# Performance work log

Measured on AMD Instinct MI355X. Metric: run time of the kernel, lower is better.

Reference implementation:

```python
import jax, jax.numpy as jnp
import numpy as np

T = 200                      # TRAIN_ROIS_PER_IMAGE
RATIO = 0.33                 # ROI_POSITIVE_RATIO
P_MAX = int(T * RATIO)       # max positive ROIs (66)
MH, MW = 28, 28              # MASK_SHAPE
STD = jnp.array([0.1, 0.1, 0.2, 0.2], jnp.float32)  # BBOX_STD_DEV
EPS = 1e-6


def _iou(a, b):
    # a [N,4], b [G,4] -> [N,G] IoU (same math as overlaps_graph, without tiling)
    ay1, ax1, ay2, ax2 = a[:, 0:1], a[:, 1:2], a[:, 2:3], a[:, 3:4]
    by1, bx1, by2, bx2 = b[None, :, 0], b[None, :, 1], b[None, :, 2], b[None, :, 3]
    iy = jnp.maximum(jnp.minimum(ay2, by2) - jnp.maximum(ay1, by1), 0.0)
    ix = jnp.maximum(jnp.minimum(ax2, bx2) - jnp.maximum(ax1, bx1), 0.0)
    inter = iy * ix
    union = (ay2 - ay1) * (ax2 - ax1) + (by2 - by1) * (bx2 - bx1) - inter
    return inter / jnp.maximum(union, EPS)


def _box_refinement(box, gt):
    # standard Mask R-CNN box_refinement_graph
    h = jnp.maximum(box[:, 2] - box[:, 0], EPS)
    w = jnp.maximum(box[:, 3] - box[:, 1], EPS)
    cy = box[:, 0] + 0.5 * h
    cx = box[:, 1] + 0.5 * w
    gh = jnp.maximum(gt[:, 2] - gt[:, 0], EPS)
    gw = jnp.maximum(gt[:, 3] - gt[:, 1], EPS)
    gcy = gt[:, 0] + 0.5 * gh
    gcx = gt[:, 1] + 0.5 * gw
    return jnp.stack([(gcy - cy) / h, (gcx - cx) / w,
                      jnp.log(gh / h), jnp.log(gw / w)], axis=-1)


def _crop_and_resize(imgs, boxes):
    # imgs [T,H,W], boxes [T,4] normalized; TF crop_and_resize bilinear semantics,
    # extrapolation_value = 0 for samples outside [0, H-1] x [0, W-1].
    Tn, H, W = imgs.shape
    y1, x1, y2, x2 = boxes[:, 0], boxes[:, 1], boxes[:, 2], boxes[:, 3]
    iy = jnp.arange(MH, dtype=jnp.float32)
    ix = jnp.arange(MW, dtype=jnp.float32)
    ys = y1[:, None] * (H - 1) + iy[None, :] * ((y2 - y1) * (H - 1) / (MH - 1))[:, None]  # [T,MH]
    xs = x1[:, None] * (W - 1) + ix[None, :] * ((x2 - x1) * (W - 1) / (MW - 1))[:, None]  # [T,MW]
    y0 = jnp.floor(ys); x0 = jnp.floor(xs)
    wy = (ys - y0)[:, :, None]
    wx = (xs - x0)[:, None, :]
    y0i = jnp.clip(y0, 0, H - 1).astype(jnp.int32)
    y1i = jnp.clip(y0 + 1, 0, H - 1).astype(jnp.int32)
    x0i = jnp.clip(x0, 0, W - 1).astype(jnp.int32)
    x1i = jnp.clip(x0 + 1, 0, W - 1).astype(jnp.int32)
    t = jnp.arange(Tn)[:, None, None]
    v00 = imgs[t, y0i[:, :, None], x0i[:, None, :]]
    v01 = imgs[t, y0i[:, :, None], x1i[:, None, :]]
    v10 = imgs[t, y1i[:, :, None], x0i[:, None, :]]
    v11 = imgs[t, y1i[:, :, None], x1i[:, None, :]]
    val = (v00 * (1 - wx) + v01 * wx) * (1 - wy) + (v10 * (1 - wx) + v11 * wx) * wy
    ok = ((ys >= 0) & (ys <= H - 1))[:, :, None] & ((xs >= 0) & (xs <= W - 1))[:, None, :]
    return jnp.where(ok, val, 0.0)


def _targets_one(proposals, class_ids, boxes, masks):
    # proposals [N,4], class_ids [G] int, boxes [G,4], masks [H,W,G]
    N = proposals.shape[0]
    # zero-padding trim expressed as validity masks (jit-friendly fixed shapes)
    valid_prop = jnp.any(proposals != 0, axis=1)
    valid_gt = jnp.any(boxes != 0, axis=1)
    non_crowd = (class_ids > 0) & valid_gt
    crowd = (class_ids < 0) & valid_gt

    ov = _iou(proposals, boxes)                              # [N,G]
    ov_nc = jnp.where(non_crowd[None, :], ov, -1.0)          # mask crowd/padded gt
    roi_iou_max = ov_nc.max(axis=1)
    crowd_max = jnp.where(crowd[None, :], ov, 0.0).max(axis=1)

    pos_mask = valid_prop & (roi_iou_max >= 0.5)
    neg_mask = valid_prop & (roi_iou_max < 0.5) & (crowd_max < 0.001)

    # deterministic selection (original uses tf.random.shuffle): positives first-in-order
    pos_order = jnp.argsort(jnp.where(pos_mask, 0, 1))
    neg_order = jnp.argsort(jnp.where(neg_mask, 0, 1))
    pos_count = jnp.minimum(pos_mask.sum(), P_MAX)
    neg_needed = jnp.floor(pos_count.astype(jnp.float32) / RATIO).astype(jnp.int32) - pos_count
    neg_count = jnp.minimum(jnp.minimum(neg_needed, neg_mask.sum()), T - pos_count)

    slot = jnp.arange(T)
    is_pos = slot < pos_count
    is_neg = (slot >= pos_count) & (slot < pos_count + neg_count)
    src = jnp.where(is_pos,
                    pos_order[jnp.clip(slot, 0, N - 1)],
                    neg_order[jnp.clip(slot - pos_count, 0, N - 1)])
    rois = jnp.where((is_pos | is_neg)[:, None], proposals[src], 0.0)

    assign = jnp.argmax(ov_nc[src], axis=1)                  # gt assignment per slot
    gt_box = boxes[assign]
    gt_cls = jnp.where(is_pos, class_ids[assign], 0)

    deltas = _box_refinement(rois, gt_box) / STD
    deltas = jnp.where(is_pos[:, None], deltas, 0.0)

    # USE_MINI_MASK: roi box in gt-box-normalized coordinates
    gy1, gx1, gy2, gx2 = gt_box[:, 0], gt_box[:, 1], gt_box[:, 2], gt_box[:, 3]
    gh = jnp.maximum(gy2 - gy1, EPS)
    gw = jnp.maximum(gx2 - gx1, EPS)
    mm = jnp.stack([(rois[:, 0] - gy1) / gh, (rois[:, 1] - gx1) / gw,
                    (rois[:, 2] - gy1) / gh, (rois[:, 3] - gx1) / gw], axis=-1)

    roi_masks = jnp.moveaxis(jnp.take(masks, assign, axis=2), 2, 0)  # [T,H,W]
    m = jnp.round(_crop_and_resize(roi_masks, mm))
    m = jnp.where(is_pos[:, None, None], m, 0.0)
    return rois, gt_cls, deltas, m


def setup_inputs() -> dict:
    key = jax.random.key(0)
    ks = jax.random.split(key, 4)
    B, N, G, HM = 16, 2000, 200, 56

    def boxes_of(k, shape):
        k1, k2, k3, k4 = jax.random.split(k, 4)
        y1 = jax.random.uniform(k1, shape) * 0.5
        x1 = jax.random.uniform(k2, shape) * 0.5
        h = 0.1 + jax.random.uniform(k3, shape) * 0.4
        w = 0.1 + jax.random.uniform(k4, shape) * 0.4
        return jnp.stack([y1, x1, y1 + h, x1 + w], axis=-1)

    proposals = boxes_of(ks[0], (B, N))
    proposals = proposals * (jnp.arange(N) < N - 200)[None, :, None]  # zero-padded tail
    prior_class_ids = jax.random.randint(ks[1], (B, G), -1, 81).astype(jnp.int32)  # -1=crowd, 0=padding
    prior_boxes = boxes_of(ks[2], (B, G)) * (prior_class_ids != 0)[..., None]
    prior_masks = (jax.random.uniform(ks[3], (B, HM, HM, G)) > 0.5).astype(jnp.float32)
    return {"proposals": proposals, "prior_class_ids": prior_class_ids,
            "prior_boxes": prior_boxes, "prior_masks": prior_masks}


def reference(proposals, prior_class_ids, prior_boxes, prior_masks):
    rois, cls, deltas, masks = jax.vmap(_targets_one)(proposals, prior_class_ids,
                                                      prior_boxes, prior_masks)
    return rois, cls, deltas, masks
```

## Files before the change

kernel.cpp:

```cpp
#include <hip/hip_runtime.h>
#include <math.h>

#pragma clang fp contract(off)

#define BN     16
#define NP     2000
#define NG     200
#define NT     200
#define PMAX   66
#define EPSF   1e-6f
#define MH     28
#define MW     28
#define HM     56
#define NPIX   (HM*HM)
#define NPLANE 66

__global__ __launch_bounds__(256) void kA(
    const float* __restrict__ proposals, const int* __restrict__ cls_ids,
    const float* __restrict__ boxes,
    int* __restrict__ flag_ws, int* __restrict__ assign_ws)
{
#pragma clang fp contract(off)
  const int b = blockIdx.y;
  __shared__ float4 gbox[NG];
  __shared__ float  garea[NG];
  __shared__ int    gflag[NG];

  for (int j = threadIdx.x; j < NG; j += 256) {
    float4 g = reinterpret_cast<const float4*>(boxes + (size_t)b * NG * 4)[j];
    int c = cls_ids[b * NG + j];
    bool vg = (g.x != 0.f) || (g.y != 0.f) || (g.z != 0.f) || (g.w != 0.f);
    gbox[j]  = g;
    garea[j] = (g.z - g.x) * (g.w - g.y);
    gflag[j] = vg ? (c > 0 ? 1 : (c < 0 ? 2 : 0)) : 0;
  }
  __syncthreads();

  int i = blockIdx.x * 256 + threadIdx.x;
  if (i >= NP) return;

  float4 p = reinterpret_cast<const float4*>(proposals + (size_t)b * NP * 4)[i];
  bool vp = (p.x != 0.f) || (p.y != 0.f) || (p.z != 0.f) || (p.w != 0.f);
  float pa = (p.z - p.x) * (p.w - p.y);

  float best = -3.0e38f;
  int   bestj = 0;
  float cmax = 0.f;
  for (int j = 0; j < NG; ++j) {
    float4 g = gbox[j];
    float iy = fmaxf(fminf(p.z, g.z) - fmaxf(p.x, g.x), 0.f);
    float ix = fmaxf(fminf(p.w, g.w) - fmaxf(p.y, g.y), 0.f);
    float inter = iy * ix;
    float uni = (pa + garea[j]) - inter;
    float iou = inter / fmaxf(uni, EPSF);
    int fl = gflag[j];
    float v = (fl == 1) ? iou : -1.0f;
    if (v > best) { best = v; bestj = j; }
    if (fl == 2) cmax = fmaxf(cmax, iou);
  }
  bool pos = vp && (best >= 0.5f);
  bool neg = vp && (best < 0.5f) && (cmax < 0.001f);
  flag_ws[b * NP + i]   = pos ? 1 : (neg ? 2 : 0);
  assign_ws[b * NP + i] = bestj;
}

__global__ __launch_bounds__(256) void kB(
    const float* __restrict__ proposals, const int* __restrict__ cls_ids,
    const float* __restrict__ boxes, const int* __restrict__ flag_ws,
    const int* __restrict__ assign_ws, float* __restrict__ out,
    float* __restrict__ mm_ws, int* __restrict__ pa_ws,
    int* __restrict__ gmap_ws)
{
#pragma clang fp contract(off)
  const int b = blockIdx.x;
  const int tid = threadIdx.x;
  const int lane = tid & 63;
  const int wv = tid >> 6;

  __shared__ unsigned short pos_list[NP];
  __shared__ unsigned short neg_list[NP];
  __shared__ int wcp[4], wcn[4];
  __shared__ int s_pt, s_nt;
  __shared__ int used[NG];
  __shared__ int gplane[NG];
  __shared__ int wtot[4];
  if (tid == 0) { s_pt = 0; s_nt = 0; }
  __syncthreads();

  const int* fb = flag_ws + b * NP;
  for (int base = 0; base < NP; base += 256) {
    int i = base + tid;
    int f = (i < NP) ? fb[i] : 0;
    bool isp = (f == 1), isn = (f == 2);
    unsigned long long bp = __ballot(isp);
    unsigned long long bn = __ballot(isn);
    __syncthreads();
    if (lane == 0) { wcp[wv] = __popcll(bp); wcn[wv] = __popcll(bn); }
    __syncthreads();
    int prep = __popcll(bp & ((1ull << lane) - 1ull));
    int pren = __popcll(bn & ((1ull << lane) - 1ull));
    int bpp = 0, bnn = 0, tp = 0, tn = 0;
    for (int w = 0; w < 4; ++w) {
      if (w < wv) { bpp += wcp[w]; bnn += wcn[w]; }
      tp += wcp[w]; tn += wcn[w];
    }
    int pt = s_pt, nt = s_nt;
    if (isp) pos_list[pt + bpp + prep] = (unsigned short)i;
    if (isn) neg_list[nt + bnn + pren] = (unsigned short)i;
    __syncthreads();
    if (tid == 0) { s_pt = pt + tp; s_nt = nt + tn; }
  }
  __syncthreads();

  int pos_total = s_pt, neg_total = s_nt;
  int pos_count = min(pos_total, PMAX);
  int neg_needed = (int)floorf((float)pos_count / 0.33f) - pos_count;
  int neg_count = min(min(neg_needed, neg_total), NT - pos_count);

  for (int j = tid; j < NG; j += 256) used[j] = 0;
  __syncthreads();

  int ma = -1;
  if (tid < NT) {
    bool ispos = tid < pos_count;
    bool isneg = (!ispos) && (tid < pos_count + neg_count);
    float r0 = 0.f, r1 = 0.f, r2 = 0.f, r3 = 0.f;
    float d0 = 0.f, d1 = 0.f, d2 = 0.f, d3 = 0.f;
    float m0 = 0.f, m1 = 0.f, m2 = 0.f, m3 = 0.f;
    float clsf = 0.f;
    if (ispos || isneg) {
      int i = ispos ? (int)pos_list[tid] : (int)neg_list[tid - pos_count];
      float4 p = reinterpret_cast<const float4*>(proposals + (size_t)b * NP * 4)[i];
      r0 = p.x; r1 = p.y; r2 = p.z; r3 = p.w;
      if (ispos) {
        int a = assign_ws[b * NP + i];
        ma = a;
        used[a] = 1;
        float4 g = reinterpret_cast<const float4*>(boxes + (size_t)b * NG * 4)[a];
        float h  = fmaxf(r2 - r0, EPSF);
        float w  = fmaxf(r3 - r1, EPSF);
        float cy = r0 + 0.5f * h;
        float cx = r1 + 0.5f * w;
        float gh = fmaxf(g.z - g.x, EPSF);
        float gw = fmaxf(g.w - g.y, EPSF);
        float gcy = g.x + 0.5f * gh;
        float gcx = g.y + 0.5f * gw;
        d0 = ((gcy - cy) / h) / 0.1f;
        d1 = ((gcx - cx) / w) / 0.1f;
        d2 = logf(gh / h) / 0.2f;
        d3 = logf(gw / w) / 0.2f;
        m0 = (r0 - g.x) / gh;
        m1 = (r1 - g.y) / gw;
        m2 = (r2 - g.x) / gh;
        m3 = (r3 - g.y) / gw;
        clsf = (float)cls_ids[b * NG + a];
      }
    }
    int s = b * NT + tid;
    float* rois = out;
    float* cls  = out + BN * NT * 4;
    float* dlt  = out + BN * NT * 4 + BN * NT;
    rois[s * 4 + 0] = r0; rois[s * 4 + 1] = r1;
    rois[s * 4 + 2] = r2; rois[s * 4 + 3] = r3;
    cls[s] = clsf;
    dlt[s * 4 + 0] = d0; dlt[s * 4 + 1] = d1;
    dlt[s * 4 + 2] = d2; dlt[s * 4 + 3] = d3;
    mm_ws[s * 4 + 0] = m0; mm_ws[s * 4 + 1] = m1;
    mm_ws[s * 4 + 2] = m2; mm_ws[s * 4 + 3] = m3;
  }
  __syncthreads();

  {
    int j = tid;
    int u = (j < NG) ? used[j] : 0;
    unsigned long long m = __ballot(u != 0);
    int pre = __popcll(m & ((1ull << lane) - 1ull));
    if (lane == 0) wtot[wv] = __popcll(m);
    __syncthreads();
    int basep = 0;
    for (int w = 0; w < wv; ++w) basep += wtot[w];
    if (j < NG) {
      int pl = u ? (basep + pre) : -1;
      gplane[j] = pl;
      gmap_ws[b * NG + j] = pl;
    }
  }
  __syncthreads();

  if (tid < NT)
    pa_ws[b * NT + tid] = (ma >= 0) ? gplane[ma] : -1;
}

__global__ __launch_bounds__(256) void kG(
    const float* __restrict__ masks, const int* __restrict__ gmap_ws,
    float* __restrict__ staged)
{
  const int b  = blockIdx.y;
  const int p0 = blockIdx.x * 64;
  const int tid = threadIdx.x;
  __shared__ float tile[64][65];
  __shared__ int   splane[64];
  __shared__ int   s_any;

  const float* mbase = masks + (size_t)b * NPIX * NG;

  for (int gc = 0; gc < NG; gc += 64) {
    if (tid < 64)
      splane[tid] = (gc + tid < NG) ? gmap_ws[b * NG + gc + tid] : -1;
    if (tid == 0) s_any = 0;
    __syncthreads();
    if (tid < 64 && splane[tid] >= 0) s_any = 1;
    __syncthreads();
    if (s_any) {
      for (int e = 0; e < 16; ++e) {
        int idx = e * 256 + tid;
        int gl  = idx & 63;
        int pl  = idx >> 6;
        int g   = gc + gl;
        float v = 0.f;
        if (g < NG) v = mbase[(size_t)(p0 + pl) * NG + g];
        tile[gl][pl] = v;
      }
      __syncthreads();
      for (int e = 0; e < 16; ++e) {
        int idx = e * 256 + tid;
        int pl  = idx & 63;
        int gl  = idx >> 6;
        int plane = splane[gl];
        if (plane >= 0)
          staged[(size_t)(b * NPLANE + plane) * NPIX + (p0 + pl)] = tile[gl][pl];
      }
    }
    __syncthreads();
  }
}

__global__ __launch_bounds__(256) void kC(
    const float* __restrict__ staged, const float* __restrict__ mm_ws,
    const int* __restrict__ pa_ws, float* __restrict__ out)
{
#pragma clang fp contract(off)
  const int s = blockIdx.x;
  float4* om = reinterpret_cast<float4*>(
      out + (size_t)(BN * NT * 9) + (size_t)s * (MH * MW));
  const int q = threadIdx.x;
  if (q >= (MH * MW) / 4) return;
  int pa = pa_ws[s];
  if (pa < 0) { om[q] = make_float4(0.f, 0.f, 0.f, 0.f); return; }

  const int b = s / NT;
  float y1 = mm_ws[s * 4 + 0], x1 = mm_ws[s * 4 + 1];
  float y2 = mm_ws[s * 4 + 2], x2 = mm_ws[s * 4 + 3];
  float sy = (y2 - y1) * 55.0f / 27.0f;
  float sx = (x2 - x1) * 55.0f / 27.0f;
  const float* mp = staged + (size_t)(b * NPLANE + pa) * NPIX;

  int px0 = q * 4;
  int my  = px0 / MW;
  float ys = y1 * 55.0f + (float)my * sy;
  float y0f = floorf(ys);
  float wy  = ys - y0f;
  int y0i = (int)fminf(fmaxf(y0f, 0.f), 55.f);
  int y1i = (int)fminf(fmaxf(y0f + 1.0f, 0.f), 55.f);
  bool oky = (ys >= 0.f) && (ys <= 55.f);
  const float* r0 = mp + y0i * HM;
  const float* r1 = mp + y1i * HM;

  float res[4];
  for (int k = 0; k < 4; ++k) {
    int mx = (px0 + k) - my * MW;
    float xs = x1 * 55.0f + (float)mx * sx;
    float x0f = floorf(xs);
    float wx  = xs - x0f;
    int x0i = (int)fminf(fmaxf(x0f, 0.f), 55.f);
    int x1i = (int)fminf(fmaxf(x0f + 1.0f, 0.f), 55.f);
    float v00 = r0[x0i], v01 = r0[x1i];
    float v10 = r1[x0i], v11 = r1[x1i];
    float val = (v00 * (1.f - wx) + v01 * wx) * (1.f - wy)
              + (v10 * (1.f - wx) + v11 * wx) * wy;
    bool ok = oky && (xs >= 0.f) && (xs <= 55.f);
    res[k] = ok ? rintf(val) : 0.f;
  }
  om[q] = make_float4(res[0], res[1], res[2], res[3]);
}

extern "C" void kernel_launch(void* const* d_in, const int* in_sizes, int n_in,
                              void* d_out, int out_size, void* d_ws, size_t ws_size,
                              hipStream_t stream)
{
  const float* proposals = (const float*)d_in[0];
  const int*   cls_ids   = (const int*)d_in[1];
  const float* boxes     = (const float*)d_in[2];
  const float* masks     = (const float*)d_in[3];
  float* out = (float*)d_out;

  char* ws = (char*)d_ws;
  int*   flag_ws   = (int*)ws;    ws += (size_t)BN * NP * sizeof(int);
  int*   assign_ws = (int*)ws;    ws += (size_t)BN * NP * sizeof(int);
  float* mm_ws     = (float*)ws;  ws += (size_t)BN * NT * 4 * sizeof(float);
  int*   pa_ws     = (int*)ws;    ws += (size_t)BN * NT * sizeof(int);
  int*   gmap_ws   = (int*)ws;    ws += (size_t)BN * NG * sizeof(int);
  float* staged    = (float*)ws;

  dim3 gA((NP + 255) / 256, BN);
  kA<<<gA, 256, 0, stream>>>(proposals, cls_ids, boxes, flag_ws, assign_ws);
  kB<<<BN, 256, 0, stream>>>(proposals, cls_ids, boxes, flag_ws, assign_ws,
                             out, mm_ws, pa_ws, gmap_ws);
  dim3 gG(NPIX / 64, BN);
  kG<<<gG, 256, 0, stream>>>(masks, gmap_ws, staged);
  kC<<<BN * NT, 256, 0, stream>>>(staged, mm_ws, pa_ws, out);
}
```

Baseline: 140.1 us.

## Rewrite mask gather with float4 row loads and compact used-plane list

The mask staging kernel now loads each 64-pixel row block of all 200 ground-truth mask values with float4 loads into a single shared tile. It then writes out only the used planes, taken from a compact list built from the plane map and a per-image used count that the selection kernel now records. This replaces the earlier loop over 64-wide GT chunks with transposes and repeated syncs. A second change lets the IoU kernel return early for zero-padded proposals. The tile is large (about 52 KB of shared memory) and the whole row block is always read, which may lower occupancy.

```diff
diff --git a/kernel.cpp b/kernel.cpp
--- a/kernel.cpp
+++ b/kernel.cpp
@@ -41,6 +41,11 @@
 
   float4 p = reinterpret_cast<const float4*>(proposals + (size_t)b * NP * 4)[i];
   bool vp = (p.x != 0.f) || (p.y != 0.f) || (p.z != 0.f) || (p.w != 0.f);
+  if (!vp) {
+    flag_ws[b * NP + i] = 0;
+    assign_ws[b * NP + i] = 0;
+    return;
+  }
   float pa = (p.z - p.x) * (p.w - p.y);
 
   float best = -3.0e38f;
@@ -58,8 +63,8 @@
     if (v > best) { best = v; bestj = j; }
     if (fl == 2) cmax = fmaxf(cmax, iou);
   }
-  bool pos = vp && (best >= 0.5f);
-  bool neg = vp && (best < 0.5f) && (cmax < 0.001f);
+  bool pos = (best >= 0.5f);
+  bool neg = (best < 0.5f) && (cmax < 0.001f);
   flag_ws[b * NP + i]   = pos ? 1 : (neg ? 2 : 0);
   assign_ws[b * NP + i] = bestj;
 }
@@ -69,7 +74,7 @@
     const float* __restrict__ boxes, const int* __restrict__ flag_ws,
     const int* __restrict__ assign_ws, float* __restrict__ out,
     float* __restrict__ mm_ws, int* __restrict__ pa_ws,
-    int* __restrict__ gmap_ws)
+    int* __restrict__ gmap_ws, int* __restrict__ ucount_ws)
 {
 #pragma clang fp contract(off)
   const int b = blockIdx.x;
@@ -187,51 +192,45 @@
   }
   __syncthreads();
 
+  if (tid == 0)
+    ucount_ws[b] = wtot[0] + wtot[1] + wtot[2] + wtot[3];
   if (tid < NT)
     pa_ws[b * NT + tid] = (ma >= 0) ? gplane[ma] : -1;
 }
 
 __global__ __launch_bounds__(256) void kG(
     const float* __restrict__ masks, const int* __restrict__ gmap_ws,
-    float* __restrict__ staged)
-{
-  const int b  = blockIdx.y;
-  const int p0 = blockIdx.x * 64;
+    const int* __restrict__ ucount_ws, float* __restrict__ staged)
+{
+  const int b   = blockIdx.y;
+  const int p0  = blockIdx.x * 64;
   const int tid = threadIdx.x;
-  __shared__ float tile[64][65];
-  __shared__ int   splane[64];
-  __shared__ int   s_any;
-
-  const float* mbase = masks + (size_t)b * NPIX * NG;
-
-  for (int gc = 0; gc < NG; gc += 64) {
-    if (tid < 64)
-      splane[tid] = (gc + tid < NG) ? gmap_ws[b * NG + gc + tid] : -1;
-    if (tid == 0) s_any = 0;
-    __syncthreads();
-    if (tid < 64 && splane[tid] >= 0) s_any = 1;
-    __syncthreads();
-    if (s_any) {
-      for (int e = 0; e < 16; ++e) {
-        int idx = e * 256 + tid;
-        int gl  = idx & 63;
-        int pl  = idx >> 6;
-        int g   = gc + gl;
-        float v = 0.f;
-        if (g < NG) v = mbase[(size_t)(p0 + pl) * NG + g];
-        tile[gl][pl] = v;
-      }
-      __syncthreads();
-      for (int e = 0; e < 16; ++e) {
-        int idx = e * 256 + tid;
-        int pl  = idx & 63;
-        int gl  = idx >> 6;
-        int plane = splane[gl];
-        if (plane >= 0)
-          staged[(size_t)(b * NPLANE + plane) * NPIX + (p0 + pl)] = tile[gl][pl];
-      }
+  const int lane = tid & 63;
+  const int wv   = tid >> 6;
+
+  __shared__ float tile[64][204];
+  __shared__ unsigned short glist[NG];
+
+  if (tid < NG) {
+    int pl = gmap_ws[b * NG + tid];
+    if (pl >= 0) glist[pl] = (unsigned short)tid;
+  }
+  const int U = ucount_ws[b];
+
+  const float* mb = masks + (size_t)b * NPIX * NG;
+  for (int r = 0; r < 16; ++r) {
+    int pl = r * 4 + wv;
+    if (lane < 50) {
+      float4 v = *reinterpret_cast<const float4*>(
+          mb + (size_t)(p0 + pl) * NG + lane * 4);
+      *reinterpret_cast<float4*>(&tile[pl][lane * 4]) = v;
     }
-    __syncthreads();
+  }
+  __syncthreads();
+
+  for (int u = wv; u < U; u += 4) {
+    int g = (int)glist[u];
+    staged[(size_t)(b * NPLANE + u) * NPIX + p0 + lane] = tile[lane][g];
   }
 }
 
@@ -300,13 +299,14 @@
   float* mm_ws     = (float*)ws;  ws += (size_t)BN * NT * 4 * sizeof(float);
   int*   pa_ws     = (int*)ws;    ws += (size_t)BN * NT * sizeof(int);
   int*   gmap_ws   = (int*)ws;    ws += (size_t)BN * NG * sizeof(int);
+  int*   ucount_ws = (int*)ws;    ws += (size_t)BN * sizeof(int);
   float* staged    = (float*)ws;
 
   dim3 gA((NP + 255) / 256, BN);
   kA<<<gA, 256, 0, stream>>>(proposals, cls_ids, boxes, flag_ws, assign_ws);
   kB<<<BN, 256, 0, stream>>>(proposals, cls_ids, boxes, flag_ws, assign_ws,
-                             out, mm_ws, pa_ws, gmap_ws);
+                             out, mm_ws, pa_ws, gmap_ws, ucount_ws);
   dim3 gG(NPIX / 64, BN);
-  kG<<<gG, 256, 0, stream>>>(masks, gmap_ws, staged);
+  kG<<<gG, 256, 0, stream>>>(masks, gmap_ws, ucount_ws, staged);
   kC<<<BN * NT, 256, 0, stream>>>(staged, mm_ws, pa_ws, out);
 }
```

Measured after the change: 130.1 us, median of 2. 1.08x faster.
